# Performance work log

Hardware: AMD Instinct MI355X
Metric: run time of the kernel (lower is better)

Reference implementation:

```python
import jax, jax.numpy as jnp
import numpy as np
from functools import partial

H = 512          # hidden_size
IN = 8 * 16      # num_features * input_size
N_LAYERS = 8
T = 4096         # rows of x -> sequence length (unbatched LSTM semantics)
OUT = 16         # fc3 output = input_size


def _uniform(key, shape, bound):
    return jax.random.uniform(key, shape, jnp.float32, -bound, bound)


def setup_inputs() -> dict:
    key = jax.random.key(0)
    ks = jax.random.split(key, 24)
    b = 1.0 / np.sqrt(H)
    inp = {
        "x": jax.random.normal(ks[0], (T, 8, 16), jnp.float32),
        # encoder layer 0 (input dim IN)
        "enc_Wih0": _uniform(ks[1], (4 * H, IN), b),
        "enc_Whh0": _uniform(ks[2], (4 * H, H), b),
        "enc_bih0": _uniform(ks[3], (4 * H,), b),
        "enc_bhh0": _uniform(ks[4], (4 * H,), b),
        # encoder layers 1..7 stacked (input dim H)
        "enc_Wih": _uniform(ks[5], (N_LAYERS - 1, 4 * H, H), b),
        "enc_Whh": _uniform(ks[6], (N_LAYERS - 1, 4 * H, H), b),
        "enc_bih": _uniform(ks[7], (N_LAYERS - 1, 4 * H), b),
        "enc_bhh": _uniform(ks[8], (N_LAYERS - 1, 4 * H), b),
        # decoder layers 0..7 stacked (input dim H)
        "dec_Wih": _uniform(ks[9], (N_LAYERS, 4 * H, H), b),
        "dec_Whh": _uniform(ks[10], (N_LAYERS, 4 * H, H), b),
        "dec_bih": _uniform(ks[11], (N_LAYERS, 4 * H), b),
        "dec_bhh": _uniform(ks[12], (N_LAYERS, 4 * H), b),
        # MLP head
        "fc1_w": _uniform(ks[13], (64, H), 1.0 / np.sqrt(H)),
        "fc1_b": _uniform(ks[14], (64,), 1.0 / np.sqrt(H)),
        "fc2_w": _uniform(ks[15], (32, 64), 1.0 / np.sqrt(64)),
        "fc2_b": _uniform(ks[16], (32,), 1.0 / np.sqrt(64)),
        "fc3_w": _uniform(ks[17], (OUT, 32), 1.0 / np.sqrt(32)),
        "fc3_b": _uniform(ks[18], (OUT,), 1.0 / np.sqrt(32)),
    }
    return inp


def _lstm_layer(seq, Wih, Whh, bih, bhh):
    # seq: (T, D_in). PyTorch gate order: i, f, g, o. Precompute input proj.
    xproj = seq @ Wih.T + bih + bhh  # (T, 4H)

    def step(carry, xp):
        h, c = carry
        g = xp + h @ Whh.T
        i, f, gg, o = jnp.split(g, 4)
        c = jax.nn.sigmoid(f) * c + jax.nn.sigmoid(i) * jnp.tanh(gg)
        h = jax.nn.sigmoid(o) * jnp.tanh(c)
        return (h, c), h

    z = jnp.zeros((H,), seq.dtype)
    _, ys = jax.lax.scan(step, (z, z), xproj)
    return ys  # (T, H)


def _stacked(seq, Wihs, Whhs, bihs, bhhs):
    # scan over the layer axis; carry is the (T, H) sequence
    def body(s, p):
        Wih, Whh, bih, bhh = p
        return _lstm_layer(s, Wih, Whh, bih, bhh), None

    s, _ = jax.lax.scan(body, seq, (Wihs, Whhs, bihs, bhhs))
    return s


def reference(x, enc_Wih0, enc_Whh0, enc_bih0, enc_bhh0,
              enc_Wih, enc_Whh, enc_bih, enc_bhh,
              dec_Wih, dec_Whh, dec_bih, dec_bhh,
              fc1_w, fc1_b, fc2_w, fc2_b, fc3_w, fc3_b):
    seq = x.reshape(x.shape[0], -1)                      # (T, IN) — unbatched LSTM input
    h = _lstm_layer(seq, enc_Wih0, enc_Whh0, enc_bih0, enc_bhh0)
    h = _stacked(h, enc_Wih, enc_Whh, enc_bih, enc_bhh)  # encoder layers 1..7
    h = _stacked(h, dec_Wih, dec_Whh, dec_bih, dec_bhh)  # decoder layers 0..7
    # MLP head (dropout = identity at inference)
    h = jax.nn.silu(h @ fc1_w.T + fc1_b)
    h = jax.nn.silu(h @ fc2_w.T + fc2_b)
    return h @ fc3_w.T + fc3_b                           # (T, OUT)
```

## Files before the change

### kernel.cpp

```cpp
#include <hip/hip_runtime.h>
#include <math.h>


#define T_SEQ 4096
#define HDIM  512
#define NL    16
#define BPL   16
#define NTH   1024
#define RING  64

typedef unsigned long long u64;
typedef _Float16 half2v __attribute__((ext_vector_type(2)));

struct Args {
  const float* x;
  const float* Wih[NL]; const float* Whh[NL];
  const float* bih[NL]; const float* bhh[NL];
  u64* ring;
  unsigned* prog;
  float* sout;
};

__device__ __forceinline__ u64 aloadU(const u64* p) {
  return __hip_atomic_load(p, __ATOMIC_RELAXED, __HIP_MEMORY_SCOPE_AGENT);
}
__device__ __forceinline__ void astoreU(u64* p, u64 v) {
  __hip_atomic_store(p, v, __ATOMIC_RELAXED, __HIP_MEMORY_SCOPE_AGENT);
}
__device__ __forceinline__ unsigned aloadu(const unsigned* p) {
  return __hip_atomic_load(p, __ATOMIC_RELAXED, __HIP_MEMORY_SCOPE_AGENT);
}
__device__ __forceinline__ float sigm(float x) { return 1.f / (1.f + __expf(-x)); }
__device__ __forceinline__ float tanhx(float x) {
  const float e = __expf(-2.f * fabsf(x));
  return copysignf((1.f - e) / (1.f + e), x);
}

#if __has_builtin(__builtin_amdgcn_fdot2)
#define DOT2(w, v, acc) __builtin_amdgcn_fdot2((w), (v), (acc), false)
#else
__device__ __forceinline__ float DOT2(half2v w, half2v v, float acc) {
  return acc + (float)w.x * (float)v.x + (float)w.y * (float)v.y;
}
#endif

#define BC(u) __builtin_bit_cast(half2v, (u))
#define DOTS8(acc, W) \
  acc = DOT2(W[0], p0, acc); acc = DOT2(W[1], p1, acc); \
  acc = DOT2(W[2], p2, acc); acc = DOT2(W[3], p3, acc); \
  acc = DOT2(W[4], p4, acc); acc = DOT2(W[5], p5, acc); \
  acc = DOT2(W[6], p6, acc); acc = DOT2(W[7], p7, acc)

__global__ void __launch_bounds__(NTH) lstm16_kernel(Args a)
{
  const int tid   = threadIdx.x;
  const int layer = blockIdx.x & 15;
  const int b     = blockIdx.x >> 4;
  const int hi    = tid >> 5;
  const int cs    = tid & 31;
  const int kx    = cs * 16;
  const int hq    = b * 32 + hi;
  const int D     = layer ? HDIM : 128;

  half2v wx[4][8], wh[4][8];
  float  bs[4];
  const bool xok = (kx + 16 <= D);
  #pragma unroll
  for (int q = 0; q < 4; ++q) {
    const int row = q * HDIM + hq;
    bs[q] = a.bih[layer][row] + a.bhh[layer][row];
    const float2* px = (const float2*)(a.Wih[layer] + (size_t)row * D + kx);
    const float2* ph = (const float2*)(a.Whh[layer] + (size_t)row * HDIM + kx);
    #pragma unroll
    for (int p = 0; p < 8; ++p) {
      const float2 t0 = xok ? px[p] : make_float2(0.f, 0.f);
      const float2 t1 = ph[p];
      half2v w0; w0.x = (_Float16)t0.x; w0.y = (_Float16)t0.y; wx[q][p] = w0;
      half2v w1; w1.x = (_Float16)t1.x; w1.y = (_Float16)t1.y; wh[q][p] = w1;
    }
  }

  __shared__ __align__(8) unsigned vx16[2][320];
  __shared__ __align__(8) unsigned vh16[320];

  u64* ringOwn        = a.ring + (size_t)layer * RING * HDIM;
  const u64* ringPrev = a.ring + (size_t)(layer ? layer - 1 : 0) * RING * HDIM;
  const unsigned* progNext = a.prog + (layer + 1) * BPL;
  unsigned* myprog         = a.prog + layer * BPL + b;

  auto stage_x = [&](int tt) {
    if (tid < 512) return;
    const int w = tid - 512;
    bool okbp = !((layer < NL - 1) && (w < 16) && ((tt & 7) == 0));
    float xv = 0.f;
    if (layer == 0) {
      if (w < 128) xv = a.x[(size_t)tt * 128 + w];
      if (!okbp)
        while ((int)aloadu(progNext + w) < tt - 40) __builtin_amdgcn_s_sleep(2);
    } else {
      const u64* xw = ringPrev + (size_t)(tt & (RING - 1)) * HDIM + w;
      u64 u = aloadU(xw);
      bool ok = ((unsigned)(u >> 32) == (unsigned)(tt + 1));
      while (!__all(ok & okbp)) {
        if (!ok) {
          u = aloadU(xw);
          ok = ((unsigned)(u >> 32) == (unsigned)(tt + 1));
          if (!ok) __builtin_amdgcn_s_sleep(1);
        }
        if (!okbp) okbp = ((int)aloadu(progNext + w) >= tt - 40);
      }
      xv = __builtin_bit_cast(float, (unsigned)(u & 0xffffffffu));
    }
    const float nb = __shfl_down(xv, 1);
    if (!(w & 1)) {
      half2v pk; pk.x = (_Float16)xv; pk.y = (_Float16)nb;
      vx16[tt & 1][(w >> 4) * 10 + ((w & 15) >> 1)] =
          __builtin_bit_cast(unsigned, pk);
    }
  };

  stage_x(0);
  __syncthreads();

  float c_state = 0.f;

  for (int t = 0; t < T_SEQ; ++t) {
    u64 hu = 0; const u64* hw = ringOwn;
    const bool hpoll = (t > 0) && (tid < 512);
    if (hpoll) {
      hw = ringOwn + (size_t)((t - 1) & (RING - 1)) * HDIM + tid;
      hu = aloadU(hw);
    }

    float a0 = 0.f, a1 = 0.f, a2 = 0.f, a3 = 0.f;
    {
      const unsigned* vb = vx16[t & 1] + cs * 10;
      const uint2 u0 = *(const uint2*)(vb + 0);
      const uint2 u1 = *(const uint2*)(vb + 2);
      const uint2 u2 = *(const uint2*)(vb + 4);
      const uint2 u3 = *(const uint2*)(vb + 6);
      const half2v p0 = BC(u0.x), p1 = BC(u0.y), p2 = BC(u1.x), p3 = BC(u1.y);
      const half2v p4 = BC(u2.x), p5 = BC(u2.y), p6 = BC(u3.x), p7 = BC(u3.y);
      DOTS8(a0, wx[0]); DOTS8(a1, wx[1]); DOTS8(a2, wx[2]); DOTS8(a3, wx[3]);
    }

    if (t > 0) {
      if (tid < 512) {
        bool ok = ((unsigned)(hu >> 32) == (unsigned)t);
        while (!__all(ok)) {
          if (!ok) { hu = aloadU(hw); ok = ((unsigned)(hu >> 32) == (unsigned)t); }
        }
        const float hv = __builtin_bit_cast(float, (unsigned)(hu & 0xffffffffu));
        const float nb = __shfl_down(hv, 1);
        if (!(tid & 1)) {
          half2v pk; pk.x = (_Float16)hv; pk.y = (_Float16)nb;
          vh16[(tid >> 4) * 10 + ((tid & 15) >> 1)] =
              __builtin_bit_cast(unsigned, pk);
        }
      }
      __syncthreads();
      {
        const unsigned* vb = vh16 + cs * 10;
        const uint2 u0 = *(const uint2*)(vb + 0);
        const uint2 u1 = *(const uint2*)(vb + 2);
        const uint2 u2 = *(const uint2*)(vb + 4);
        const uint2 u3 = *(const uint2*)(vb + 6);
        const half2v p0 = BC(u0.x), p1 = BC(u0.y), p2 = BC(u1.x), p3 = BC(u1.y);
        const half2v p4 = BC(u2.x), p5 = BC(u2.y), p6 = BC(u3.x), p7 = BC(u3.y);
        DOTS8(a0, wh[0]); DOTS8(a1, wh[1]); DOTS8(a2, wh[2]); DOTS8(a3, wh[3]);
      }
    }

    #pragma unroll
    for (int d = 1; d < 32; d <<= 1) {
      a0 += __shfl_xor(a0, d); a1 += __shfl_xor(a1, d);
      a2 += __shfl_xor(a2, d); a3 += __shfl_xor(a3, d);
    }

    if (cs == 0) {
      const float gi = sigm(a0 + bs[0]);
      const float gf = sigm(a1 + bs[1]);
      const float gg = tanhx(a2 + bs[2]);
      const float go = sigm(a3 + bs[3]);
      c_state = gf * c_state + gi * gg;
      const float h = go * tanhx(c_state);
      astoreU(ringOwn + (size_t)(t & (RING - 1)) * HDIM + hq,
              ((u64)(unsigned)(t + 1) << 32) | (u64)__builtin_bit_cast(unsigned, h));
      if (layer == NL - 1) a.sout[(size_t)t * HDIM + hq] = h;
    }
    if (tid == 0 && (t & 7) == 7)
      __hip_atomic_store(myprog, (unsigned)(t + 1), __ATOMIC_RELAXED,
                         __HIP_MEMORY_SCOPE_AGENT);

    if (t + 1 < T_SEQ) stage_x(t + 1);
    __syncthreads();
  }
}

__global__ void __launch_bounds__(64) mlp_head_kernel(
    const float* __restrict__ S,
    const float* __restrict__ w1, const float* __restrict__ b1,
    const float* __restrict__ w2, const float* __restrict__ b2,
    const float* __restrict__ w3, const float* __restrict__ b3,
    float* __restrict__ out)
{
  const int r   = blockIdx.x;
  const int tid = threadIdx.x;
  __shared__ __align__(16) float hbuf[HDIM];
  __shared__ float a1[64];
  __shared__ float a2[32];

  #pragma unroll
  for (int u = 0; u < HDIM / 64; ++u)
    hbuf[u * 64 + tid] = S[(size_t)r * HDIM + u * 64 + tid];
  __syncthreads();

  float acc = b1[tid];
  {
    const float4* w4 = (const float4*)(w1 + (size_t)tid * HDIM);
    const float4* h4 = (const float4*)hbuf;
    #pragma unroll 8
    for (int k = 0; k < HDIM / 4; ++k) {
      const float4 wv = w4[k], hv = h4[k];
      acc = fmaf(wv.x, hv.x, acc); acc = fmaf(wv.y, hv.y, acc);
      acc = fmaf(wv.z, hv.z, acc); acc = fmaf(wv.w, hv.w, acc);
    }
  }
  a1[tid] = acc * sigm(acc);
  __syncthreads();

  if (tid < 32) {
    float acc2 = b2[tid];
    #pragma unroll
    for (int k = 0; k < 64; ++k) acc2 = fmaf(a1[k], w2[tid * 64 + k], acc2);
    a2[tid] = acc2 * sigm(acc2);
  }
  __syncthreads();

  if (tid < 16) {
    float acc3 = b3[tid];
    #pragma unroll
    for (int k = 0; k < 32; ++k) acc3 = fmaf(a2[k], w3[tid * 32 + k], acc3);
    out[(size_t)r * 16 + tid] = acc3;
  }
}

extern "C" void kernel_launch(void* const* d_in, const int* in_sizes, int n_in,
                              void* d_out, int out_size, void* d_ws, size_t ws_size,
                              hipStream_t stream)
{
  (void)in_sizes; (void)n_in; (void)out_size; (void)ws_size;

  const float* x     = (const float*)d_in[0];
  const float* eWih0 = (const float*)d_in[1];
  const float* eWhh0 = (const float*)d_in[2];
  const float* ebih0 = (const float*)d_in[3];
  const float* ebhh0 = (const float*)d_in[4];
  const float* eWih  = (const float*)d_in[5];
  const float* eWhh  = (const float*)d_in[6];
  const float* ebih  = (const float*)d_in[7];
  const float* ebhh  = (const float*)d_in[8];
  const float* dWih  = (const float*)d_in[9];
  const float* dWhh  = (const float*)d_in[10];
  const float* dbih  = (const float*)d_in[11];
  const float* dbhh  = (const float*)d_in[12];
  const float* fc1w  = (const float*)d_in[13];
  const float* fc1b  = (const float*)d_in[14];
  const float* fc2w  = (const float*)d_in[15];
  const float* fc2b  = (const float*)d_in[16];
  const float* fc3w  = (const float*)d_in[17];
  const float* fc3b  = (const float*)d_in[18];
  float* out = (float*)d_out;

  const size_t RINGBYTES = (size_t)NL * RING * HDIM * sizeof(u64);
  Args p{};
  p.x    = x;
  p.ring = (u64*)d_ws;
  p.prog = (unsigned*)((char*)d_ws + RINGBYTES);
  p.sout = (float*)((char*)d_ws + RINGBYTES + 4096);

  p.Wih[0] = eWih0; p.Whh[0] = eWhh0; p.bih[0] = ebih0; p.bhh[0] = ebhh0;
  for (int l = 1; l < 8; ++l) {
    p.Wih[l] = eWih + (size_t)(l - 1) * 4 * HDIM * HDIM;
    p.Whh[l] = eWhh + (size_t)(l - 1) * 4 * HDIM * HDIM;
    p.bih[l] = ebih + (size_t)(l - 1) * 4 * HDIM;
    p.bhh[l] = ebhh + (size_t)(l - 1) * 4 * HDIM;
  }
  for (int l = 8; l < 16; ++l) {
    p.Wih[l] = dWih + (size_t)(l - 8) * 4 * HDIM * HDIM;
    p.Whh[l] = dWhh + (size_t)(l - 8) * 4 * HDIM * HDIM;
    p.bih[l] = dbih + (size_t)(l - 8) * 4 * HDIM;
    p.bhh[l] = dbhh + (size_t)(l - 8) * 4 * HDIM;
  }

  hipMemsetAsync(d_ws, 0, RINGBYTES + 4096, stream);

  void* args[] = { &p };
  hipError_t e = hipLaunchCooperativeKernel((const void*)lstm16_kernel,
                                            dim3(NL * BPL), dim3(NTH), args, 0,
                                            stream);
  if (e != hipSuccess)
    lstm16_kernel<<<dim3(NL * BPL), dim3(NTH), 0, stream>>>(p);

  mlp_head_kernel<<<dim3(T_SEQ), dim3(64), 0, stream>>>(
      p.sout, fc1w, fc1b, fc2w, fc2b, fc3w, fc3b, out);
}
```

Before: 9.241 ms.

## Pack fp16 hidden pairs into ring slots and cut per-step barriers to one

Producers now pack two fp16 hidden values into each ring entry, which halves the number of ring words (256 per step instead of 512) that consumers poll and removes the shuffle-and-pack step on the read side. The hidden-state staging buffer is double-buffered and the next-x staging is moved before a single barrier, so each timestep uses one __syncthreads instead of two. Every lane now computes the gate activations redundantly so that lane pairs can be shuffled into a packed store. The cost is more redundant transcendental work per step, and the ring values are now fp16, which drops fp32 precision in the inter-layer data.

```diff
diff --git a/kernel.cpp b/kernel.cpp
--- a/kernel.cpp
+++ b/kernel.cpp
@@ -8,6 +8,8 @@
 #define BPL   16
 #define NTH   1024
 #define RING  64
+#define RMASK 63
+#define RW    256
 
 typedef unsigned long long u64;
 typedef _Float16 half2v __attribute__((ext_vector_type(2)));
@@ -51,7 +53,7 @@
   acc = DOT2(W[4], p4, acc); acc = DOT2(W[5], p5, acc); \
   acc = DOT2(W[6], p6, acc); acc = DOT2(W[7], p7, acc)
 
-__global__ void __launch_bounds__(NTH) lstm16_kernel(Args a)
+__global__ void __launch_bounds__(NTH, 4) lstm16_kernel(Args a)
 {
   const int tid   = threadIdx.x;
   const int layer = blockIdx.x & 15;
@@ -81,24 +83,29 @@
   }
 
   __shared__ __align__(8) unsigned vx16[2][320];
-  __shared__ __align__(8) unsigned vh16[320];
-
-  u64* ringOwn        = a.ring + (size_t)layer * RING * HDIM;
-  const u64* ringPrev = a.ring + (size_t)(layer ? layer - 1 : 0) * RING * HDIM;
+  __shared__ __align__(8) unsigned vh16[2][320];
+
+  u64* ringOwn        = a.ring + (size_t)layer * RING * RW;
+  const u64* ringPrev = a.ring + (size_t)(layer ? layer - 1 : 0) * RING * RW;
   const unsigned* progNext = a.prog + (layer + 1) * BPL;
   unsigned* myprog         = a.prog + layer * BPL + b;
 
   auto stage_x = [&](int tt) {
     if (tid < 512) return;
     const int w = tid - 512;
-    bool okbp = !((layer < NL - 1) && (w < 16) && ((tt & 7) == 0));
-    float xv = 0.f;
+    if (w >= RW) return;
+    const int dst = (w >> 3) * 10 + (w & 7);
     if (layer == 0) {
-      if (w < 128) xv = a.x[(size_t)tt * 128 + w];
-      if (!okbp)
+      if (w < 64) {
+        const float2 xv = *(const float2*)(a.x + (size_t)tt * 128 + 2 * w);
+        half2v pk; pk.x = (_Float16)xv.x; pk.y = (_Float16)xv.y;
+        vx16[tt & 1][dst] = __builtin_bit_cast(unsigned, pk);
+      }
+      if ((layer < NL - 1) && (w < BPL) && ((tt & 7) == 0))
         while ((int)aloadu(progNext + w) < tt - 40) __builtin_amdgcn_s_sleep(2);
     } else {
-      const u64* xw = ringPrev + (size_t)(tt & (RING - 1)) * HDIM + w;
+      const u64* xw = ringPrev + (size_t)(tt & RMASK) * RW + w;
+      bool okbp = !((layer < NL - 1) && (w < BPL) && ((tt & 7) == 0));
       u64 u = aloadU(xw);
       bool ok = ((unsigned)(u >> 32) == (unsigned)(tt + 1));
       while (!__all(ok & okbp)) {
@@ -109,26 +116,25 @@
         }
         if (!okbp) okbp = ((int)aloadu(progNext + w) >= tt - 40);
       }
-      xv = __builtin_bit_cast(float, (unsigned)(u & 0xffffffffu));
-    }
-    const float nb = __shfl_down(xv, 1);
-    if (!(w & 1)) {
-      half2v pk; pk.x = (_Float16)xv; pk.y = (_Float16)nb;
-      vx16[tt & 1][(w >> 4) * 10 + ((w & 15) >> 1)] =
-          __builtin_bit_cast(unsigned, pk);
+      vx16[tt & 1][dst] = (unsigned)u;
     }
   };
 
+  for (int i = tid; i < 640; i += NTH) {
+    ((unsigned*)vx16)[i] = 0;
+    ((unsigned*)vh16)[i] = 0;
+  }
+  __syncthreads();
   stage_x(0);
   __syncthreads();
 
-  float c_state = 0.f;
+  float cst = 0.f;
 
   for (int t = 0; t < T_SEQ; ++t) {
     u64 hu = 0; const u64* hw = ringOwn;
-    const bool hpoll = (t > 0) && (tid < 512);
-    if (hpoll) {
-      hw = ringOwn + (size_t)((t - 1) & (RING - 1)) * HDIM + tid;
+    const bool hp = (t > 0) && (tid < RW);
+    if (hp) {
+      hw = ringOwn + (size_t)((t - 1) & RMASK) * RW + tid;
       hu = aloadU(hw);
     }
 
@@ -144,31 +150,27 @@
       DOTS8(a0, wx[0]); DOTS8(a1, wx[1]); DOTS8(a2, wx[2]); DOTS8(a3, wx[3]);
     }
 
+    if (hp) {
+      bool ok = ((unsigned)(hu >> 32) == (unsigned)t);
+      while (!__all(ok)) {
+        if (!ok) { hu = aloadU(hw); ok = ((unsigned)(hu >> 32) == (unsigned)t); }
+      }
+      vh16[t & 1][(tid >> 3) * 10 + (tid & 7)] = (unsigned)hu;
+    }
+
+    if (t + 1 < T_SEQ) stage_x(t + 1);
+
+    __syncthreads();
+
     if (t > 0) {
-      if (tid < 512) {
-        bool ok = ((unsigned)(hu >> 32) == (unsigned)t);
-        while (!__all(ok)) {
-          if (!ok) { hu = aloadU(hw); ok = ((unsigned)(hu >> 32) == (unsigned)t); }
-        }
-        const float hv = __builtin_bit_cast(float, (unsigned)(hu & 0xffffffffu));
-        const float nb = __shfl_down(hv, 1);
-        if (!(tid & 1)) {
-          half2v pk; pk.x = (_Float16)hv; pk.y = (_Float16)nb;
-          vh16[(tid >> 4) * 10 + ((tid & 15) >> 1)] =
-              __builtin_bit_cast(unsigned, pk);
-        }
-      }
-      __syncthreads();
-      {
-        const unsigned* vb = vh16 + cs * 10;
-        const uint2 u0 = *(const uint2*)(vb + 0);
-        const uint2 u1 = *(const uint2*)(vb + 2);
-        const uint2 u2 = *(const uint2*)(vb + 4);
-        const uint2 u3 = *(const uint2*)(vb + 6);
-        const half2v p0 = BC(u0.x), p1 = BC(u0.y), p2 = BC(u1.x), p3 = BC(u1.y);
-        const half2v p4 = BC(u2.x), p5 = BC(u2.y), p6 = BC(u3.x), p7 = BC(u3.y);
-        DOTS8(a0, wh[0]); DOTS8(a1, wh[1]); DOTS8(a2, wh[2]); DOTS8(a3, wh[3]);
-      }
+      const unsigned* vb = vh16[t & 1] + cs * 10;
+      const uint2 u0 = *(const uint2*)(vb + 0);
+      const uint2 u1 = *(const uint2*)(vb + 2);
+      const uint2 u2 = *(const uint2*)(vb + 4);
+      const uint2 u3 = *(const uint2*)(vb + 6);
+      const half2v p0 = BC(u0.x), p1 = BC(u0.y), p2 = BC(u1.x), p3 = BC(u1.y);
+      const half2v p4 = BC(u2.x), p5 = BC(u2.y), p6 = BC(u3.x), p7 = BC(u3.y);
+      DOTS8(a0, wh[0]); DOTS8(a1, wh[1]); DOTS8(a2, wh[2]); DOTS8(a3, wh[3]);
     }
 
     #pragma unroll
@@ -177,23 +179,26 @@
       a2 += __shfl_xor(a2, d); a3 += __shfl_xor(a3, d);
     }
 
-    if (cs == 0) {
-      const float gi = sigm(a0 + bs[0]);
-      const float gf = sigm(a1 + bs[1]);
-      const float gg = tanhx(a2 + bs[2]);
-      const float go = sigm(a3 + bs[3]);
-      c_state = gf * c_state + gi * gg;
-      const float h = go * tanhx(c_state);
-      astoreU(ringOwn + (size_t)(t & (RING - 1)) * HDIM + hq,
-              ((u64)(unsigned)(t + 1) << 32) | (u64)__builtin_bit_cast(unsigned, h));
-      if (layer == NL - 1) a.sout[(size_t)t * HDIM + hq] = h;
-    }
+    const float gi = sigm(a0 + bs[0]);
+    const float gf = sigm(a1 + bs[1]);
+    const float gg = tanhx(a2 + bs[2]);
+    const float go = sigm(a3 + bs[3]);
+    cst = gf * cst + gi * gg;
+    const float h = go * tanhx(cst);
+
+    const unsigned hu16 =
+        (unsigned)__builtin_bit_cast(unsigned short, (_Float16)h);
+    const unsigned other = __shfl_down(hu16, 32);
+    if ((tid & 63) == 0) {
+      const unsigned pay = hu16 | (other << 16);
+      astoreU(ringOwn + (size_t)(t & RMASK) * RW + (b * 16 + (tid >> 6)),
+              ((u64)(unsigned)(t + 1) << 32) | (u64)pay);
+    }
+    if (layer == NL - 1 && (tid & 31) == 0)
+      a.sout[(size_t)t * HDIM + hq] = h;
     if (tid == 0 && (t & 7) == 7)
       __hip_atomic_store(myprog, (unsigned)(t + 1), __ATOMIC_RELAXED,
                          __HIP_MEMORY_SCOPE_AGENT);
-
-    if (t + 1 < T_SEQ) stage_x(t + 1);
-    __syncthreads();
   }
 }
 
@@ -272,7 +277,7 @@
   const float* fc3b  = (const float*)d_in[18];
   float* out = (float*)d_out;
 
-  const size_t RINGBYTES = (size_t)NL * RING * HDIM * sizeof(u64);
+  const size_t RINGBYTES = (size_t)NL * RING * RW * sizeof(u64);
   Args p{};
   p.x    = x;
   p.ring = (u64*)d_ws;
```

After: 17.07 ms. 84.7% more time.

## Poll hidden-state ring with 16-byte sc1 loads and prefetch next input early

Applied to the files above, without the earlier changes.

The own-layer h poll now reads the ring with 256 threads using inline-asm global_load_dwordx4 with the sc1 cache bit. Each thread takes two (value,tag) pairs and packs them straight into the fp16 shared buffer, so the shuffle step goes away and fewer memory requests are issued. The next-timestep x/ring load and the backpressure wait move to the top of the loop, so their latency overlaps with the dot products; the tag check is deferred until after the gate math. This adds inline asm with a manual vmcnt wait and sched_barrier. It also relies on a 16-byte load returning both tags consistently.

```diff
diff --git a/kernel.cpp b/kernel.cpp
--- a/kernel.cpp
+++ b/kernel.cpp
@@ -35,6 +35,14 @@
   const float e = __expf(-2.f * fabsf(x));
   return copysignf((1.f - e) / (1.f + e), x);
 }
+
+#define HP_ISSUE(r, p) \
+  asm volatile("global_load_dwordx4 %0, %1, off sc1" : "=v"(r) : "v"(p))
+#define HP_WAIT()                                          \
+  do {                                                     \
+    asm volatile("s_waitcnt vmcnt(0)" ::: "memory");       \
+    __builtin_amdgcn_sched_barrier(0);                     \
+  } while (0)
 
 #if __has_builtin(__builtin_amdgcn_fdot2)
 #define DOT2(w, v, acc) __builtin_amdgcn_fdot2((w), (v), (acc), false)
@@ -88,48 +96,58 @@
   const unsigned* progNext = a.prog + (layer + 1) * BPL;
   unsigned* myprog         = a.prog + layer * BPL + b;
 
-  auto stage_x = [&](int tt) {
+  auto stage_x0 = [&]() {
     if (tid < 512) return;
     const int w = tid - 512;
-    bool okbp = !((layer < NL - 1) && (w < 16) && ((tt & 7) == 0));
     float xv = 0.f;
     if (layer == 0) {
-      if (w < 128) xv = a.x[(size_t)tt * 128 + w];
-      if (!okbp)
-        while ((int)aloadu(progNext + w) < tt - 40) __builtin_amdgcn_s_sleep(2);
+      if (w < 128) xv = a.x[w];
     } else {
-      const u64* xw = ringPrev + (size_t)(tt & (RING - 1)) * HDIM + w;
+      const u64* xw = ringPrev + w;
       u64 u = aloadU(xw);
-      bool ok = ((unsigned)(u >> 32) == (unsigned)(tt + 1));
-      while (!__all(ok & okbp)) {
+      bool ok = ((unsigned)(u >> 32) == 1u);
+      while (!__all(ok)) {
         if (!ok) {
           u = aloadU(xw);
-          ok = ((unsigned)(u >> 32) == (unsigned)(tt + 1));
+          ok = ((unsigned)(u >> 32) == 1u);
           if (!ok) __builtin_amdgcn_s_sleep(1);
         }
-        if (!okbp) okbp = ((int)aloadu(progNext + w) >= tt - 40);
       }
       xv = __builtin_bit_cast(float, (unsigned)(u & 0xffffffffu));
     }
     const float nb = __shfl_down(xv, 1);
     if (!(w & 1)) {
       half2v pk; pk.x = (_Float16)xv; pk.y = (_Float16)nb;
-      vx16[tt & 1][(w >> 4) * 10 + ((w & 15) >> 1)] =
-          __builtin_bit_cast(unsigned, pk);
+      vx16[0][(w >> 4) * 10 + ((w & 15) >> 1)] = __builtin_bit_cast(unsigned, pk);
     }
   };
 
-  stage_x(0);
+  stage_x0();
   __syncthreads();
 
   float c_state = 0.f;
 
   for (int t = 0; t < T_SEQ; ++t) {
-    u64 hu = 0; const u64* hw = ringOwn;
-    const bool hpoll = (t > 0) && (tid < 512);
-    if (hpoll) {
-      hw = ringOwn + (size_t)((t - 1) & (RING - 1)) * HDIM + tid;
-      hu = aloadU(hw);
+    uint4 raw = make_uint4(0, 0, 0, 0);
+    const bool hpoll = (t > 0) && (tid < 256);
+    const uint4* hw4 =
+        (const uint4*)(ringOwn + (size_t)((t - 1) & (RING - 1)) * HDIM) + tid;
+    if (hpoll) HP_ISSUE(raw, hw4);
+
+    u64 xu = 0; const u64* xw = ringPrev;
+    float xv0 = 0.f;
+    const bool xio = (tid >= 512) && (t + 1 < T_SEQ);
+    if (xio) {
+      const int w = tid - 512;
+      if (layer == 0) {
+        if (w < 128) xv0 = a.x[(size_t)(t + 1) * 128 + w];
+      } else {
+        xw = ringPrev + (size_t)((t + 1) & (RING - 1)) * HDIM + w;
+        xu = aloadU(xw);
+      }
+      if ((layer < NL - 1) && (w < 16) && (((t + 1) & 7) == 0))
+        while ((int)aloadu(progNext + w) < t + 1 - 40)
+          __builtin_amdgcn_s_sleep(2);
     }
 
     float a0 = 0.f, a1 = 0.f, a2 = 0.f, a3 = 0.f;
@@ -145,18 +163,21 @@
     }
 
     if (t > 0) {
-      if (tid < 512) {
-        bool ok = ((unsigned)(hu >> 32) == (unsigned)t);
+      if (tid < 256) {
+        HP_WAIT();
+        bool ok = (raw.y == (unsigned)t) && (raw.w == (unsigned)t);
         while (!__all(ok)) {
-          if (!ok) { hu = aloadU(hw); ok = ((unsigned)(hu >> 32) == (unsigned)t); }
+          if (!ok) {
+            __builtin_amdgcn_s_sleep(1);
+            HP_ISSUE(raw, hw4);
+            HP_WAIT();
+            ok = (raw.y == (unsigned)t) && (raw.w == (unsigned)t);
+          }
         }
-        const float hv = __builtin_bit_cast(float, (unsigned)(hu & 0xffffffffu));
-        const float nb = __shfl_down(hv, 1);
-        if (!(tid & 1)) {
-          half2v pk; pk.x = (_Float16)hv; pk.y = (_Float16)nb;
-          vh16[(tid >> 4) * 10 + ((tid & 15) >> 1)] =
-              __builtin_bit_cast(unsigned, pk);
-        }
+        const float h0 = __builtin_bit_cast(float, raw.x);
+        const float h1 = __builtin_bit_cast(float, raw.z);
+        half2v pk; pk.x = (_Float16)h0; pk.y = (_Float16)h1;
+        vh16[(tid >> 3) * 10 + (tid & 7)] = __builtin_bit_cast(unsigned, pk);
       }
       __syncthreads();
       {
@@ -192,7 +213,29 @@
       __hip_atomic_store(myprog, (unsigned)(t + 1), __ATOMIC_RELAXED,
                          __HIP_MEMORY_SCOPE_AGENT);
 
-    if (t + 1 < T_SEQ) stage_x(t + 1);
+    if (xio) {
+      const int w = tid - 512;
+      float xv;
+      if (layer == 0) {
+        xv = xv0;
+      } else {
+        bool ok = ((unsigned)(xu >> 32) == (unsigned)(t + 2));
+        while (!__all(ok)) {
+          if (!ok) {
+            xu = aloadU(xw);
+            ok = ((unsigned)(xu >> 32) == (unsigned)(t + 2));
+            if (!ok) __builtin_amdgcn_s_sleep(1);
+          }
+        }
+        xv = __builtin_bit_cast(float, (unsigned)(xu & 0xffffffffu));
+      }
+      const float nb = __shfl_down(xv, 1);
+      if (!(w & 1)) {
+        half2v pk; pk.x = (_Float16)xv; pk.y = (_Float16)nb;
+        vx16[(t + 1) & 1][(w >> 4) * 10 + ((w & 15) >> 1)] =
+            __builtin_bit_cast(unsigned, pk);
+      }
+    }
     __syncthreads();
   }
 }
@@ -293,7 +336,7 @@
     p.bhh[l] = dbhh + (size_t)(l - 8) * 4 * HDIM;
   }
 
-  hipMemsetAsync(d_ws, 0, RINGBYTES + 4096, stream);
+  (void)hipMemsetAsync(d_ws, 0, RINGBYTES + 4096, stream);
 
   void* args[] = { &p };
   hipError_t e = hipLaunchCooperativeKernel((const void*)lstm16_kernel,
```

New measurement: 9.340 ms. About the same (+1.1%).
